# Optimization experiments

Measured on AMD Instinct MI355X. Metric: run time of the kernel, lower is better.

Reference implementation:

```python
import jax, jax.numpy as jnp
import numpy as np

N_NODES = 65536
N_EDGES = 1048576
IN_FEATS = 128
H1 = 128
H2 = 256
N_CLASSES = 16


def setup_inputs() -> dict:
    key = jax.random.key(0)
    ks = jax.random.split(key, 12)
    s = 0.05
    x = jax.random.normal(ks[0], (N_NODES, IN_FEATS), dtype=jnp.float32)
    src = jax.random.randint(ks[1], (N_EDGES,), 0, N_NODES, dtype=jnp.int32)
    dst = jax.random.randint(ks[2], (N_EDGES,), 0, N_NODES, dtype=jnp.int32)
    # SAGEConv('pool') params: fc_pool (bias), fc_self (no bias), fc_neigh (no bias), output bias
    Wp = jax.random.normal(ks[3], (H1, IN_FEATS), dtype=jnp.float32) * s
    bp = jnp.zeros((H1,), dtype=jnp.float32)
    Ws = jax.random.normal(ks[4], (H1, IN_FEATS), dtype=jnp.float32) * s
    Wn = jax.random.normal(ks[5], (H1, H1), dtype=jnp.float32) * s
    bn = jnp.zeros((H1,), dtype=jnp.float32)
    # MLP head
    W1 = jax.random.normal(ks[6], (H2, H1), dtype=jnp.float32) * s
    b1 = jnp.zeros((H2,), dtype=jnp.float32)
    W2 = jax.random.normal(ks[7], (N_CLASSES, H2), dtype=jnp.float32) * s
    b2 = jnp.zeros((N_CLASSES,), dtype=jnp.float32)
    return {"x": x, "Wp": Wp, "bp": bp, "Ws": Ws, "Wn": Wn, "bn": bn,
            "W1": W1, "b1": b1, "W2": W2, "b2": b2, "src": src, "dst": dst}


def reference(x, Wp, bp, Ws, Wn, bn, W1, b1, W2, b2, src, dst):
    N = x.shape[0]
    # SAGEConv 'pool': per-edge MLP on gathered source features, segment-max over dst
    m = jax.nn.relu(x[src] @ Wp.T + bp)              # [E, H1]
    pooled = jax.ops.segment_max(m, dst, num_segments=N)  # [N, H1], -inf for isolated
    pooled = jnp.where(jnp.isneginf(pooled), 0.0, pooled)
    h = x @ Ws.T + pooled @ Wn.T + bn                # combine self + neigh
    h = jax.nn.leaky_relu(h)                         # slope 0.01 matches torch default
    h = jax.nn.leaky_relu(h @ W1.T + b1)
    # dropout is identity in eval mode
    h = jax.nn.sigmoid(h @ W2.T + b2)
    return h
```

## Files before the change

### kernel.cpp

```cpp
#include <hip/hip_runtime.h>
#include <cstdint>
#include <cstddef>

typedef __attribute__((ext_vector_type(8))) __bf16 bf16x8;
typedef __attribute__((ext_vector_type(4))) float f32x4;

static __device__ __forceinline__ unsigned short f2b(float f) {
    union { float f; unsigned int u; } v; v.f = f;
    unsigned int u = v.u;
    unsigned int r = (u + 0x7fffu + ((u >> 16) & 1u)) >> 16;
    return (unsigned short)r;
}

template<int K, int ACT>
__global__ __launch_bounds__(256) void mfma_gemm(
    const unsigned short* __restrict__ A, int strideA,
    const unsigned short* __restrict__ W,
    const float* __restrict__ bias,
    unsigned short* __restrict__ C, int Ncols)
{
    const int nt = Ncols >> 7;
    const int bm = (int)blockIdx.x / nt, bn = (int)blockIdx.x % nt;
    const int w  = threadIdx.x >> 6;
    const int wm = w & 1, wn = w >> 1;
    const int l  = threadIdx.x & 63;
    const int lr = l & 15, quad = l >> 4;
    const int m0 = bm * 128 + wm * 64;
    const int n0 = bn * 128 + wn * 64;

    f32x4 acc[4][4];
#pragma unroll
    for (int i = 0; i < 4; i++)
#pragma unroll
        for (int j = 0; j < 4; j++) acc[i][j] = (f32x4){0.f, 0.f, 0.f, 0.f};

    const unsigned short* Ap = A + (size_t)(m0 + lr) * strideA + quad * 8;
    const unsigned short* Bp = W + (size_t)(n0 + lr) * K + quad * 8;

    for (int ks = 0; ks < K / 32; ks++) {
        bf16x8 af[4], bf[4];
#pragma unroll
        for (int i = 0; i < 4; i++)
            af[i] = *(const bf16x8*)(Ap + (size_t)i * 16 * strideA + ks * 32);
#pragma unroll
        for (int i = 0; i < 4; i++)
            bf[i] = *(const bf16x8*)(Bp + (size_t)i * 16 * K + ks * 32);
#pragma unroll
        for (int mi = 0; mi < 4; mi++)
#pragma unroll
            for (int ni = 0; ni < 4; ni++)
                acc[mi][ni] = __builtin_amdgcn_mfma_f32_16x16x32_bf16(
                    af[mi], bf[ni], acc[mi][ni], 0, 0, 0);
    }

#pragma unroll
    for (int ni = 0; ni < 4; ni++) {
        const int col = n0 + ni * 16 + lr;
        const float bv = bias[col];
#pragma unroll
        for (int mi = 0; mi < 4; mi++) {
#pragma unroll
            for (int r = 0; r < 4; r++) {
                const int row = m0 + mi * 16 + quad * 4 + r;
                float v = acc[mi][ni][r] + bv;
                if (ACT == 1) v = v > 0.f ? v : 0.f;
                if (ACT == 2) v = v > 0.f ? v : 0.01f * v;
                C[(size_t)row * Ncols + col] = f2b(v);
            }
        }
    }
}

__global__ __launch_bounds__(256) void head_mfma(
    const unsigned short* __restrict__ H, const unsigned short* __restrict__ W2b,
    const float* __restrict__ b2, float* __restrict__ out)
{
    const int wave = (int)(blockIdx.x * 4) + (threadIdx.x >> 6);
    const int l = threadIdx.x & 63;
    const int lr = l & 15, quad = l >> 4;
    const int m0 = wave * 16;
    f32x4 acc = (f32x4){0.f, 0.f, 0.f, 0.f};
#pragma unroll
    for (int ks = 0; ks < 8; ks++) {
        bf16x8 a = *(const bf16x8*)(H + (size_t)(m0 + lr) * 256 + ks * 32 + quad * 8);
        bf16x8 b = *(const bf16x8*)(W2b + (size_t)lr * 256 + ks * 32 + quad * 8);
        acc = __builtin_amdgcn_mfma_f32_16x16x32_bf16(a, b, acc, 0, 0, 0);
    }
    const float bv = b2[lr];
#pragma unroll
    for (int r = 0; r < 4; r++) {
        const int row = m0 + quad * 4 + r;
        float v = acc[r] + bv;
        out[(size_t)row * 16 + lr] = 1.f / (1.f + __expf(-v));
    }
}

__global__ __launch_bounds__(256) void conv_x_kernel(
    const float* __restrict__ x, unsigned short* __restrict__ bufX, int total)
{
    int t = blockIdx.x * 256 + threadIdx.x;
    if (t >= total) return;
    int row = t >> 5, seg = t & 31;
    float4 v = *(const float4*)(x + (size_t)row * 128 + seg * 4);
    ushort4 o;
    o.x = f2b(v.x); o.y = f2b(v.y); o.z = f2b(v.z); o.w = f2b(v.w);
    *(ushort4*)(bufX + (size_t)row * 256 + seg * 4) = o;
}

__global__ __launch_bounds__(256) void conv_w_kernel(
    const float* __restrict__ Wp, const float* __restrict__ Ws,
    const float* __restrict__ Wn, const float* __restrict__ W1,
    const float* __restrict__ W2,
    unsigned short* __restrict__ Wp_b, unsigned short* __restrict__ Wcat,
    unsigned short* __restrict__ W1_b, unsigned short* __restrict__ W2_b)
{
    int i = blockIdx.x * 256 + threadIdx.x;
    if (i < 16384) {
        Wp_b[i] = f2b(Wp[i]);
    } else if (i < 49152) {
        int j = i - 16384; int o = j >> 8, k = j & 255;
        Wcat[j] = f2b(k < 128 ? Ws[o * 128 + k] : Wn[o * 128 + (k - 128)]);
    } else if (i < 81920) {
        W1_b[i - 49152] = f2b(W1[i - 49152]);
    } else if (i < 86016) {
        W2_b[i - 81920] = f2b(W2[i - 81920]);
    }
}

__global__ __launch_bounds__(256) void bucket_count(
    const int* __restrict__ dst, int* __restrict__ bcnt, int E)
{
    __shared__ int h[1024];
    for (int i = threadIdx.x; i < 1024; i += 256) h[i] = 0;
    __syncthreads();
    int base = blockIdx.x * 4096;
#pragma unroll
    for (int i = 0; i < 16; i++) {
        int e = base + i * 256 + threadIdx.x;
        if (e < E) atomicAdd(&h[((unsigned)dst[e]) >> 6], 1);
    }
    __syncthreads();
    for (int i = threadIdx.x; i < 1024; i += 256)
        if (h[i]) atomicAdd(&bcnt[i], h[i]);
}

__global__ __launch_bounds__(1024) void bucket_scan(
    const int* __restrict__ bcnt, int* __restrict__ boff, int* __restrict__ bcur)
{
    __shared__ int s[1024];
    int t = threadIdx.x;
    s[t] = bcnt[t];
    __syncthreads();
    for (int d = 1; d < 1024; d <<= 1) {
        int add = (t >= d) ? s[t - d] : 0;
        __syncthreads();
        s[t] += add;
        __syncthreads();
    }
    int ex = (t == 0) ? 0 : s[t - 1];
    boff[t] = ex; bcur[t] = ex;
    if (t == 1023) boff[1024] = s[1023];
}

__global__ __launch_bounds__(256) void bucket_scatter(
    const int* __restrict__ src, const int* __restrict__ dst,
    int* __restrict__ bcur, unsigned int* __restrict__ pairs, int E)
{
    __shared__ int h[1024];
    __shared__ int base_l[1024];
    __shared__ int cnt[1024];
    for (int i = threadIdx.x; i < 1024; i += 256) { h[i] = 0; cnt[i] = 0; }
    __syncthreads();
    int base = blockIdx.x * 4096;
    int d_r[16], s_r[16];
#pragma unroll
    for (int i = 0; i < 16; i++) {
        int e = base + i * 256 + threadIdx.x;
        if (e < E) {
            d_r[i] = dst[e]; s_r[i] = src[e];
            atomicAdd(&h[((unsigned)d_r[i]) >> 6], 1);
        } else d_r[i] = -1;
    }
    __syncthreads();
    for (int i = threadIdx.x; i < 1024; i += 256)
        base_l[i] = h[i] ? atomicAdd(&bcur[i], h[i]) : 0;
    __syncthreads();
#pragma unroll
    for (int i = 0; i < 16; i++) {
        if (d_r[i] >= 0) {
            int b = ((unsigned)d_r[i]) >> 6;
            int pos = base_l[b] + atomicAdd(&cnt[b], 1);
            pairs[pos] = ((unsigned)s_r[i] << 6) | ((unsigned)d_r[i] & 63u);
        }
    }
}

__global__ __launch_bounds__(256) void bucket_pool2(
    const unsigned int* __restrict__ yu, const int* __restrict__ boff,
    const unsigned int* __restrict__ pairs, unsigned short* __restrict__ bufX)
{
    __shared__ unsigned short ldsSrc[3072];
    __shared__ int bin[64], offl[64], cnt2[64];
    const int b = blockIdx.x;
    const int tid = threadIdx.x;
    if (tid < 64) { bin[tid] = 0; cnt2[tid] = 0; }
    __syncthreads();
    const int beg = boff[b];
    const int nb = boff[b + 1] - beg;

    for (int i = tid; i < nb; i += 256)
        atomicAdd(&bin[pairs[beg + i] & 63u], 1);
    __syncthreads();
    if (tid == 0) {
        int run = 0;
        for (int i = 0; i < 64; i++) { offl[i] = run; run += bin[i]; }
    }
    __syncthreads();
    for (int i = tid; i < nb; i += 256) {
        unsigned int p = pairs[beg + i];
        int d = p & 63u;
        int slot = offl[d] + atomicAdd(&cnt2[d], 1);
        ldsSrc[slot] = (unsigned short)(p >> 6);
    }
    __syncthreads();

    const int w = tid >> 6, lane = tid & 63;
    for (int ni = 0; ni < 16; ni++) {
        const int n = w * 16 + ni;
        const int e0 = offl[n], cnt = bin[n];
        float ax = 0.f, ay = 0.f;
        for (int e = 0; e < cnt; e += 8) {
            int s[8]; unsigned int v[8];
#pragma unroll
            for (int j = 0; j < 8; j++) {
                int idx = e + j; idx = idx < cnt ? idx : cnt - 1;
                s[j] = ldsSrc[e0 + idx];
            }
#pragma unroll
            for (int j = 0; j < 8; j++) v[j] = yu[(size_t)s[j] * 64 + lane];
#pragma unroll
            for (int j = 0; j < 8; j++) {
                ax = fmaxf(ax, __uint_as_float(v[j] << 16));
                ay = fmaxf(ay, __uint_as_float(v[j] & 0xffff0000u));
            }
        }
        unsigned int packed = (__float_as_uint(ax) >> 16) | (__float_as_uint(ay) & 0xffff0000u);
        ((unsigned int*)bufX)[(size_t)(b * 64 + n) * 128 + 64 + lane] = packed;
    }
}

extern "C" void kernel_launch(void* const* d_in, const int* in_sizes, int n_in,
                              void* d_out, int out_size, void* d_ws, size_t ws_size,
                              hipStream_t stream)
{
    const float* x  = (const float*)d_in[0];
    const float* Wp = (const float*)d_in[1];
    const float* bp = (const float*)d_in[2];
    const float* Ws = (const float*)d_in[3];
    const float* Wn = (const float*)d_in[4];
    const float* bn = (const float*)d_in[5];
    const float* W1 = (const float*)d_in[6];
    const float* b1 = (const float*)d_in[7];
    const float* W2 = (const float*)d_in[8];
    const float* b2 = (const float*)d_in[9];
    const int* src  = (const int*)d_in[10];
    const int* dst  = (const int*)d_in[11];
    float* out = (float*)d_out;

    const int N = in_sizes[0] / 128;
    const int E = in_sizes[10];

    unsigned short* bufX = (unsigned short*)d_ws;
    unsigned short* y    = (unsigned short*)((char*)d_ws + (size_t)32 * 1024 * 1024);
    unsigned short* hbuf = (unsigned short*)((char*)d_ws + (size_t)48 * 1024 * 1024);
    unsigned short* h2   = (unsigned short*)((char*)d_ws + (size_t)64 * 1024 * 1024);

    unsigned short* Wp_b = (unsigned short*)((char*)d_ws + (size_t)96 * 1024 * 1024);
    unsigned short* Wcat = Wp_b + 16384;
    unsigned short* W1_b = Wcat + 32768;
    unsigned short* W2_b = W1_b + 32768;
    int* bcnt = (int*)(W2_b + 4096);
    int* boff = bcnt + 1024;
    int* bcur = boff + 1025 + 3;
    unsigned int* pairs = (unsigned int*)(bcur + 1024);

    dim3 blk(256);

    conv_w_kernel<<<(86016 + 255) / 256, blk, 0, stream>>>(
        Wp, Ws, Wn, W1, W2, Wp_b, Wcat, W1_b, W2_b);
    conv_x_kernel<<<(N * 32 + 255) / 256, blk, 0, stream>>>(x, bufX, N * 32);

    hipMemsetAsync(bcnt, 0, 1024 * sizeof(int), stream);
    const int ebks = (E + 4095) / 4096;
    bucket_count<<<ebks, blk, 0, stream>>>(dst, bcnt, E);
    bucket_scan<<<1, 1024, 0, stream>>>(bcnt, boff, bcur);
    bucket_scatter<<<ebks, blk, 0, stream>>>(src, dst, bcur, pairs, E);

    mfma_gemm<128, 1><<<(N / 128) * 1, blk, 0, stream>>>(
        bufX, 256, Wp_b, bp, y, 128);

    bucket_pool2<<<1024, blk, 0, stream>>>((const unsigned int*)y, boff, pairs, bufX);

    mfma_gemm<256, 2><<<(N / 128) * 1, blk, 0, stream>>>(
        bufX, 256, Wcat, bn, hbuf, 128);

    mfma_gemm<128, 2><<<(N / 128) * 2, blk, 0, stream>>>(
        hbuf, 128, W1_b, b1, h2, 256);

    head_mfma<<<N / 64, blk, 0, stream>>>(h2, W2_b, b2, out);
}
```

Measured before the change: 238.2 us.

## Fuse x conversion into first GEMM, merge weight conversion, use 32-node buckets

Converts x to bf16 inside the first MFMA GEMM, writing the bf16 copy to bufX while computing y, which removes a separate conversion pass. Weight conversion is folded into the bucket counting kernel to save a launch. Destination buckets shrink from 64 to 32 nodes, doubling the pooling blocks for better occupancy and load balance. The cost is more global atomics and a larger scan, and each fused GEMM block reads x as fp32.

```diff
diff --git a/kernel.cpp b/kernel.cpp
--- a/kernel.cpp
+++ b/kernel.cpp
@@ -4,6 +4,8 @@
 
 typedef __attribute__((ext_vector_type(8))) __bf16 bf16x8;
 typedef __attribute__((ext_vector_type(4))) float f32x4;
+
+union bf8pack { unsigned short u[8]; bf16x8 v; uint4 q; };
 
 static __device__ __forceinline__ unsigned short f2b(float f) {
     union { float f; unsigned int u; } v; v.f = f;
@@ -71,6 +73,73 @@
     }
 }
 
+__global__ __launch_bounds__(256) void k1_fused(
+    const float* __restrict__ x, const unsigned short* __restrict__ Wp_b,
+    const float* __restrict__ bias, unsigned short* __restrict__ bufX,
+    unsigned short* __restrict__ y)
+{
+    const int bm = blockIdx.x;
+    const int w  = threadIdx.x >> 6;
+    const int wm = w & 1, wn = w >> 1;
+    const int l  = threadIdx.x & 63;
+    const int lr = l & 15, quad = l >> 4;
+    const int m0 = bm * 128 + wm * 64;
+    const int n0 = wn * 64;
+
+    f32x4 acc[4][4];
+#pragma unroll
+    for (int i = 0; i < 4; i++)
+#pragma unroll
+        for (int j = 0; j < 4; j++) acc[i][j] = (f32x4){0.f, 0.f, 0.f, 0.f};
+
+    const float* Ap = x + (size_t)(m0 + lr) * 128 + quad * 8;
+    const unsigned short* Bp = Wp_b + (size_t)(n0 + lr) * 128 + quad * 8;
+
+#pragma unroll
+    for (int ks = 0; ks < 4; ks++) {
+        bf16x8 af[4], bf[4];
+#pragma unroll
+        for (int i = 0; i < 4; i++) {
+            const float* p = Ap + (size_t)i * 16 * 128 + ks * 32;
+            float4 f0 = *(const float4*)p;
+            float4 f1 = *(const float4*)(p + 4);
+            bf8pack pk;
+            pk.u[0] = f2b(f0.x); pk.u[1] = f2b(f0.y);
+            pk.u[2] = f2b(f0.z); pk.u[3] = f2b(f0.w);
+            pk.u[4] = f2b(f1.x); pk.u[5] = f2b(f1.y);
+            pk.u[6] = f2b(f1.z); pk.u[7] = f2b(f1.w);
+            af[i] = pk.v;
+            if (wn == 0)
+                *(uint4*)(bufX + (size_t)(m0 + lr + i * 16) * 256 + ks * 32 + quad * 8) = pk.q;
+        }
+#pragma unroll
+        for (int i = 0; i < 4; i++)
+            bf[i] = *(const bf16x8*)(Bp + (size_t)i * 16 * 128 + ks * 32);
+#pragma unroll
+        for (int mi = 0; mi < 4; mi++)
+#pragma unroll
+            for (int ni = 0; ni < 4; ni++)
+                acc[mi][ni] = __builtin_amdgcn_mfma_f32_16x16x32_bf16(
+                    af[mi], bf[ni], acc[mi][ni], 0, 0, 0);
+    }
+
+#pragma unroll
+    for (int ni = 0; ni < 4; ni++) {
+        const int col = n0 + ni * 16 + lr;
+        const float bv = bias[col];
+#pragma unroll
+        for (int mi = 0; mi < 4; mi++) {
+#pragma unroll
+            for (int r = 0; r < 4; r++) {
+                const int row = m0 + mi * 16 + quad * 4 + r;
+                float v = acc[mi][ni][r] + bv;
+                v = v > 0.f ? v : 0.f;
+                y[(size_t)row * 128 + col] = f2b(v);
+            }
+        }
+    }
+}
+
 __global__ __launch_bounds__(256) void head_mfma(
     const unsigned short* __restrict__ H, const unsigned short* __restrict__ W2b,
     const float* __restrict__ b2, float* __restrict__ out)
@@ -95,52 +164,39 @@
     }
 }
 
-__global__ __launch_bounds__(256) void conv_x_kernel(
-    const float* __restrict__ x, unsigned short* __restrict__ bufX, int total)
-{
-    int t = blockIdx.x * 256 + threadIdx.x;
-    if (t >= total) return;
-    int row = t >> 5, seg = t & 31;
-    float4 v = *(const float4*)(x + (size_t)row * 128 + seg * 4);
-    ushort4 o;
-    o.x = f2b(v.x); o.y = f2b(v.y); o.z = f2b(v.z); o.w = f2b(v.w);
-    *(ushort4*)(bufX + (size_t)row * 256 + seg * 4) = o;
-}
-
-__global__ __launch_bounds__(256) void conv_w_kernel(
+__global__ __launch_bounds__(256) void count_conv(
+    const int* __restrict__ dst, int* __restrict__ bcnt, int E, int ebks,
     const float* __restrict__ Wp, const float* __restrict__ Ws,
     const float* __restrict__ Wn, const float* __restrict__ W1,
     const float* __restrict__ W2,
     unsigned short* __restrict__ Wp_b, unsigned short* __restrict__ Wcat,
     unsigned short* __restrict__ W1_b, unsigned short* __restrict__ W2_b)
 {
-    int i = blockIdx.x * 256 + threadIdx.x;
-    if (i < 16384) {
-        Wp_b[i] = f2b(Wp[i]);
-    } else if (i < 49152) {
-        int j = i - 16384; int o = j >> 8, k = j & 255;
-        Wcat[j] = f2b(k < 128 ? Ws[o * 128 + k] : Wn[o * 128 + (k - 128)]);
-    } else if (i < 81920) {
-        W1_b[i - 49152] = f2b(W1[i - 49152]);
-    } else if (i < 86016) {
-        W2_b[i - 81920] = f2b(W2[i - 81920]);
-    }
-}
-
-__global__ __launch_bounds__(256) void bucket_count(
-    const int* __restrict__ dst, int* __restrict__ bcnt, int E)
-{
-    __shared__ int h[1024];
-    for (int i = threadIdx.x; i < 1024; i += 256) h[i] = 0;
+    if ((int)blockIdx.x >= ebks) {
+        int i = ((int)blockIdx.x - ebks) * 256 + threadIdx.x;
+        if (i < 16384) {
+            Wp_b[i] = f2b(Wp[i]);
+        } else if (i < 49152) {
+            int j = i - 16384; int o = j >> 8, k = j & 255;
+            Wcat[j] = f2b(k < 128 ? Ws[o * 128 + k] : Wn[o * 128 + (k - 128)]);
+        } else if (i < 81920) {
+            W1_b[i - 49152] = f2b(W1[i - 49152]);
+        } else if (i < 86016) {
+            W2_b[i - 81920] = f2b(W2[i - 81920]);
+        }
+        return;
+    }
+    __shared__ int h[2048];
+    for (int i = threadIdx.x; i < 2048; i += 256) h[i] = 0;
     __syncthreads();
     int base = blockIdx.x * 4096;
 #pragma unroll
     for (int i = 0; i < 16; i++) {
         int e = base + i * 256 + threadIdx.x;
-        if (e < E) atomicAdd(&h[((unsigned)dst[e]) >> 6], 1);
-    }
-    __syncthreads();
-    for (int i = threadIdx.x; i < 1024; i += 256)
+        if (e < E) atomicAdd(&h[((unsigned)dst[e]) >> 5], 1);
+    }
+    __syncthreads();
+    for (int i = threadIdx.x; i < 2048; i += 256)
         if (h[i]) atomicAdd(&bcnt[i], h[i]);
 }
 
@@ -149,7 +205,8 @@
 {
     __shared__ int s[1024];
     int t = threadIdx.x;
-    s[t] = bcnt[t];
+    int c0 = bcnt[2 * t], c1 = bcnt[2 * t + 1];
+    s[t] = c0 + c1;
     __syncthreads();
     for (int d = 1; d < 1024; d <<= 1) {
         int add = (t >= d) ? s[t - d] : 0;
@@ -158,18 +215,19 @@
         __syncthreads();
     }
     int ex = (t == 0) ? 0 : s[t - 1];
-    boff[t] = ex; bcur[t] = ex;
-    if (t == 1023) boff[1024] = s[1023];
+    boff[2 * t] = ex;          bcur[2 * t] = ex;
+    boff[2 * t + 1] = ex + c0; bcur[2 * t + 1] = ex + c0;
+    if (t == 1023) boff[2048] = s[1023];
 }
 
 __global__ __launch_bounds__(256) void bucket_scatter(
     const int* __restrict__ src, const int* __restrict__ dst,
     int* __restrict__ bcur, unsigned int* __restrict__ pairs, int E)
 {
-    __shared__ int h[1024];
-    __shared__ int base_l[1024];
-    __shared__ int cnt[1024];
-    for (int i = threadIdx.x; i < 1024; i += 256) { h[i] = 0; cnt[i] = 0; }
+    __shared__ int h[2048];
+    __shared__ int base_l[2048];
+    __shared__ int cnt[2048];
+    for (int i = threadIdx.x; i < 2048; i += 256) { h[i] = 0; cnt[i] = 0; }
     __syncthreads();
     int base = blockIdx.x * 4096;
     int d_r[16], s_r[16];
@@ -178,55 +236,55 @@
         int e = base + i * 256 + threadIdx.x;
         if (e < E) {
             d_r[i] = dst[e]; s_r[i] = src[e];
-            atomicAdd(&h[((unsigned)d_r[i]) >> 6], 1);
+            atomicAdd(&h[((unsigned)d_r[i]) >> 5], 1);
         } else d_r[i] = -1;
     }
     __syncthreads();
-    for (int i = threadIdx.x; i < 1024; i += 256)
+    for (int i = threadIdx.x; i < 2048; i += 256)
         base_l[i] = h[i] ? atomicAdd(&bcur[i], h[i]) : 0;
     __syncthreads();
 #pragma unroll
     for (int i = 0; i < 16; i++) {
         if (d_r[i] >= 0) {
-            int b = ((unsigned)d_r[i]) >> 6;
+            int b = ((unsigned)d_r[i]) >> 5;
             int pos = base_l[b] + atomicAdd(&cnt[b], 1);
-            pairs[pos] = ((unsigned)s_r[i] << 6) | ((unsigned)d_r[i] & 63u);
-        }
-    }
-}
-
-__global__ __launch_bounds__(256) void bucket_pool2(
+            pairs[pos] = ((unsigned)s_r[i] << 5) | ((unsigned)d_r[i] & 31u);
+        }
+    }
+}
+
+__global__ __launch_bounds__(256) void bucket_pool3(
     const unsigned int* __restrict__ yu, const int* __restrict__ boff,
     const unsigned int* __restrict__ pairs, unsigned short* __restrict__ bufX)
 {
-    __shared__ unsigned short ldsSrc[3072];
-    __shared__ int bin[64], offl[64], cnt2[64];
+    __shared__ unsigned short ldsSrc[2048];
+    __shared__ int bin[32], offl[32], cnt2[32];
     const int b = blockIdx.x;
     const int tid = threadIdx.x;
-    if (tid < 64) { bin[tid] = 0; cnt2[tid] = 0; }
+    if (tid < 32) { bin[tid] = 0; cnt2[tid] = 0; }
     __syncthreads();
     const int beg = boff[b];
     const int nb = boff[b + 1] - beg;
 
     for (int i = tid; i < nb; i += 256)
-        atomicAdd(&bin[pairs[beg + i] & 63u], 1);
+        atomicAdd(&bin[pairs[beg + i] & 31u], 1);
     __syncthreads();
     if (tid == 0) {
         int run = 0;
-        for (int i = 0; i < 64; i++) { offl[i] = run; run += bin[i]; }
+        for (int i = 0; i < 32; i++) { offl[i] = run; run += bin[i]; }
     }
     __syncthreads();
     for (int i = tid; i < nb; i += 256) {
         unsigned int p = pairs[beg + i];
-        int d = p & 63u;
+        int d = p & 31u;
         int slot = offl[d] + atomicAdd(&cnt2[d], 1);
-        ldsSrc[slot] = (unsigned short)(p >> 6);
+        ldsSrc[slot] = (unsigned short)(p >> 5);
     }
     __syncthreads();
 
     const int w = tid >> 6, lane = tid & 63;
-    for (int ni = 0; ni < 16; ni++) {
-        const int n = w * 16 + ni;
+    for (int ni = 0; ni < 8; ni++) {
+        const int n = w * 8 + ni;
         const int e0 = offl[n], cnt = bin[n];
         float ax = 0.f, ay = 0.f;
         for (int e = 0; e < cnt; e += 8) {
@@ -245,7 +303,7 @@
             }
         }
         unsigned int packed = (__float_as_uint(ax) >> 16) | (__float_as_uint(ay) & 0xffff0000u);
-        ((unsigned int*)bufX)[(size_t)(b * 64 + n) * 128 + 64 + lane] = packed;
+        ((unsigned int*)bufX)[(size_t)(b * 32 + n) * 128 + 64 + lane] = packed;
     }
 }
 
@@ -280,26 +338,23 @@
     unsigned short* W1_b = Wcat + 32768;
     unsigned short* W2_b = W1_b + 32768;
     int* bcnt = (int*)(W2_b + 4096);
-    int* boff = bcnt + 1024;
-    int* bcur = boff + 1025 + 3;
-    unsigned int* pairs = (unsigned int*)(bcur + 1024);
+    int* boff = bcnt + 2048;
+    int* bcur = boff + 2049 + 3;
+    unsigned int* pairs = (unsigned int*)(bcur + 2048);
 
     dim3 blk(256);
-
-    conv_w_kernel<<<(86016 + 255) / 256, blk, 0, stream>>>(
-        Wp, Ws, Wn, W1, W2, Wp_b, Wcat, W1_b, W2_b);
-    conv_x_kernel<<<(N * 32 + 255) / 256, blk, 0, stream>>>(x, bufX, N * 32);
-
-    hipMemsetAsync(bcnt, 0, 1024 * sizeof(int), stream);
     const int ebks = (E + 4095) / 4096;
-    bucket_count<<<ebks, blk, 0, stream>>>(dst, bcnt, E);
+    const int cbks = (86016 + 255) / 256;
+
+    hipMemsetAsync(bcnt, 0, 2048 * sizeof(int), stream);
+    count_conv<<<ebks + cbks, blk, 0, stream>>>(
+        dst, bcnt, E, ebks, Wp, Ws, Wn, W1, W2, Wp_b, Wcat, W1_b, W2_b);
     bucket_scan<<<1, 1024, 0, stream>>>(bcnt, boff, bcur);
     bucket_scatter<<<ebks, blk, 0, stream>>>(src, dst, bcur, pairs, E);
 
-    mfma_gemm<128, 1><<<(N / 128) * 1, blk, 0, stream>>>(
-        bufX, 256, Wp_b, bp, y, 128);
-
-    bucket_pool2<<<1024, blk, 0, stream>>>((const unsigned int*)y, boff, pairs, bufX);
+    k1_fused<<<N / 128, blk, 0, stream>>>(x, Wp_b, bp, bufX, y);
+
+    bucket_pool3<<<2048, blk, 0, stream>>>((const unsigned int*)y, boff, pairs, bufX);
 
     mfma_gemm<256, 2><<<(N / 128) * 1, blk, 0, stream>>>(
         bufX, 256, Wcat, bn, hbuf, 128);
```

After: 243.1 us. 2.1% more time.
